# Kernel tuning notes

Measured on AMD Instinct MI355X. Metric: run time of the kernel, lower is better.

## Reference

```python
import jax, jax.numpy as jnp
import numpy as np

N, E, B = 50000, 800000, 16
IN_DIM, ED, HD, SD, NC = 64, 8, 128, 128, 8
T_STEPS = (8 + 16) // 2  # eval mode: (t_min + t_max) // 2 = 12


def setup_inputs() -> dict:
    key = jax.random.key(0)
    ks = jax.random.split(key, 12)
    s = 0.05  # small init scale so 12 residual steps stay bounded
    return {
        "x": jax.random.normal(ks[0], (N, IN_DIM), jnp.float32),
        "edge_index": jax.random.randint(ks[1], (2, E), 0, N, jnp.int64),
        "edge_attr": jax.random.normal(ks[2], (E, ED), jnp.float32),
        "batch": jnp.sort(jax.random.randint(ks[3], (N,), 0, B, jnp.int64)),
        "enc_w": jax.random.normal(ks[4], (IN_DIM, SD), jnp.float32) * s,
        "enc_b": jnp.zeros((SD,), jnp.float32),
        "msg_w": jax.random.normal(ks[5], (SD + ED, HD), jnp.float32) * s,
        "msg_b": jnp.zeros((HD,), jnp.float32),
        "up_w1": jax.random.normal(ks[6], (SD + HD, HD), jnp.float32) * s,
        "up_b1": jnp.zeros((HD,), jnp.float32),
        "up_w2": jax.random.normal(ks[7], (HD, SD), jnp.float32) * s,
        "up_b2": jnp.zeros((SD,), jnp.float32),
    }


def reference(x, edge_index, edge_attr, batch, enc_w, enc_b, msg_w, msg_b,
              up_w1, up_b1, up_w2, up_b2):
    src, dst = edge_index[0], edge_index[1]  # x_j = x[src], aggregate at dst
    # in-degree for mean aggregation (zero-degree nodes get 0, clamp avoids /0)
    deg = jax.ops.segment_sum(jnp.ones((E,), x.dtype), dst, num_segments=N)
    deg = jnp.clip(deg, 1.0)[:, None]

    # Encoder: Linear + ReLU
    state = jax.nn.relu(x @ enc_w + enc_b)  # [N, SD]

    for _ in range(T_STEPS):
        # message: relu(W_msg @ [h_j || e_ji])
        m = jax.nn.relu(jnp.concatenate([state[src], edge_attr], axis=-1) @ msg_w + msg_b)  # [E, HD]
        agg = jax.ops.segment_sum(m, dst, num_segments=N) / deg  # scatter-mean [N, HD]
        # update MLP on [h_i || m_bar_i]
        h = jax.nn.relu(jnp.concatenate([state, agg], axis=-1) @ up_w1 + up_b1)
        delta = h @ up_w2 + up_b2
        state = state + delta  # eval: no stochastic mask, no noise

    # Readout: per-graph mean over class channels
    class_ch = state[:, -NC:]  # [N, NC]
    cnt = jax.ops.segment_sum(jnp.ones((N,), x.dtype), batch, num_segments=B)
    logits = jax.ops.segment_sum(class_ch, batch, num_segments=B) / jnp.clip(cnt, 1.0)[:, None]
    return logits
```

## Files before the change

kernel.cpp:

```cpp
#include <hip/hip_runtime.h>
#include <hip/hip_bf16.h>

#define NN 50000
#define NE 800000
#define NB 16
#define T_STEPS 12
#define SCAN_B 196
#define EAW_BLOCKS 2048

typedef __attribute__((ext_vector_type(8))) short short8;
typedef __attribute__((ext_vector_type(4))) float f32x4;
typedef __attribute__((ext_vector_type(2))) float f32x2;
typedef unsigned short u16;
typedef unsigned int u32;

__device__ __forceinline__ float bf2f(u32 u) {
    union { u32 i; float f; } v; v.i = u << 16; return v.f;
}
__device__ __forceinline__ u16 f2bf(float f) {
    union { float f; u32 i; } v; v.f = f;
    u32 r = v.i + 0x7fffu + ((v.i >> 16) & 1u);
    return (u16)(r >> 16);
}
__device__ __forceinline__ f32x4 mfma16(short8 a, short8 b, f32x4 c) {
    return __builtin_amdgcn_mfma_f32_16x16x32_bf16(a, b, c, 0, 0, 0);
}

__device__ __forceinline__ u32 pk2_fp8(float o0, float o1) {
#if __has_builtin(__builtin_amdgcn_cvt_pk_fp8_f32)
    return (u32)__builtin_amdgcn_cvt_pk_fp8_f32(o0, o1, 0, false);
#else
    u32 a = 0;
    asm("v_cvt_pk_fp8_f32 %0, %1, %2" : "+v"(a) : "v"(o0), "v"(o1));
    return a;
#endif
}
__device__ __forceinline__ u32 pk4_fp8(float o0, float o1, float o2, float o3) {
    return (pk2_fp8(o0, o1) & 0xffffu) | (pk2_fp8(o2, o3) << 16);
}

__device__ __forceinline__ void fp8x4f(u32 w, float& f0, float& f1, float& f2, float& f3) {
#if __has_builtin(__builtin_amdgcn_cvt_pk_f32_fp8)
    f32x2 r0 = __builtin_amdgcn_cvt_pk_f32_fp8((int)w, false);
    f32x2 r1 = __builtin_amdgcn_cvt_pk_f32_fp8((int)w, true);
    f0 = r0[0]; f1 = r0[1]; f2 = r1[0]; f3 = r1[1];
#else
    f32x2 r0, r1;
    u32 hi = w >> 16;
    asm("v_cvt_pk_f32_fp8 %0, %1" : "=v"(r0) : "v"(w));
    asm("v_cvt_pk_f32_fp8 %0, %1" : "=v"(r1) : "v"(hi));
    f0 = r0[0]; f1 = r0[1]; f2 = r1[0]; f3 = r1[1];
#endif
}

#define W1OFF 0
#define W2OFF 32768
#define WSOFF 49152
#define ENCOFF 65536
#define PACKN 73728


__global__ void k_hist(const int* __restrict__ dst, int* __restrict__ hist) {
    int e = blockIdx.x * 256 + threadIdx.x;
    if (e < NE) atomicAdd(&hist[dst[e]], 1);
}

__global__ void k_scanA(const int* __restrict__ hist, int* __restrict__ excl,
                        int* __restrict__ bsum) {
    __shared__ int sh[256];
    int t = threadIdx.x, b = blockIdx.x;
    int idx = b * 256 + t;
    int v = (idx < NN) ? hist[idx] : 0;
    sh[t] = v;
    __syncthreads();
    for (int off = 1; off < 256; off <<= 1) {
        int add = (t >= off) ? sh[t - off] : 0;
        __syncthreads();
        sh[t] += add;
        __syncthreads();
    }
    if (idx < NN) excl[idx] = sh[t] - v;
    if (t == 255) bsum[b] = sh[255];
}

__global__ void k_scanB(int* __restrict__ bsum) {
    __shared__ int sh[256];
    int t = threadIdx.x;
    int v = (t < SCAN_B) ? bsum[t] : 0;
    sh[t] = v;
    __syncthreads();
    for (int off = 1; off < 256; off <<= 1) {
        int add = (t >= off) ? sh[t - off] : 0;
        __syncthreads();
        sh[t] += add;
        __syncthreads();
    }
    if (t < SCAN_B) bsum[t] = sh[t] - v;
}

__global__ void k_scanC(const int* __restrict__ excl, const int* __restrict__ bsum,
                        int* __restrict__ rowptr, int* __restrict__ cursor) {
    int idx = blockIdx.x * 256 + threadIdx.x;
    if (idx < NN) {
        int r = excl[idx] + bsum[blockIdx.x];
        rowptr[idx] = r;
        cursor[idx] = r;
    }
    if (idx == 0) rowptr[NN] = NE;
}

__global__ void k_scatter(const int* __restrict__ src, const int* __restrict__ dst,
                          const float* __restrict__ eattr, int* __restrict__ cursor,
                          int* __restrict__ ssrc, u16* __restrict__ ea8) {
    int e = blockIdx.x * 256 + threadIdx.x;
    if (e >= NE) return;
    int d = dst[e];
    int pos = atomicAdd(&cursor[d], 1);
    ssrc[pos] = src[e];
    const float* ap = eattr + (size_t)e * 8;
    uint4 w;
    w.x = (u32)f2bf(ap[0]) | ((u32)f2bf(ap[1]) << 16);
    w.y = (u32)f2bf(ap[2]) | ((u32)f2bf(ap[3]) << 16);
    w.z = (u32)f2bf(ap[4]) | ((u32)f2bf(ap[5]) << 16);
    w.w = (u32)f2bf(ap[6]) | ((u32)f2bf(ap[7]) << 16);
    *(uint4*)(ea8 + (size_t)pos * 8) = w;
}

__global__ __launch_bounds__(256) void k_eaw(
    const u16* __restrict__ ea8, const float* __restrict__ msg_w,
    unsigned char* __restrict__ eaw) {
    const int tid = threadIdx.x;
    const int hex = tid & 15;
    const int esub = tid >> 4;
    float w[8][8];
#pragma unroll
    for (int k = 0; k < 8; ++k) {
        float4 v0 = *(const float4*)(msg_w + (size_t)(128 + k) * 128 + hex * 8);
        float4 v1 = *(const float4*)(msg_w + (size_t)(128 + k) * 128 + hex * 8 + 4);
        w[k][0] = v0.x; w[k][1] = v0.y; w[k][2] = v0.z; w[k][3] = v0.w;
        w[k][4] = v1.x; w[k][5] = v1.y; w[k][6] = v1.z; w[k][7] = v1.w;
    }
    int p = blockIdx.x * 16 + esub;
    if (p >= NE) return;
    uint4 ev = *(const uint4*)(ea8 + (size_t)p * 8);
    while (true) {
        int pn = p + EAW_BLOCKS * 16;
        bool more = pn < NE;
        uint4 evn;
        if (more) evn = *(const uint4*)(ea8 + (size_t)pn * 8);
        float ef[8];
        ef[0] = bf2f(ev.x & 0xffffu); ef[1] = bf2f(ev.x >> 16);
        ef[2] = bf2f(ev.y & 0xffffu); ef[3] = bf2f(ev.y >> 16);
        ef[4] = bf2f(ev.z & 0xffffu); ef[5] = bf2f(ev.z >> 16);
        ef[6] = bf2f(ev.w & 0xffffu); ef[7] = bf2f(ev.w >> 16);
        float o[8];
#pragma unroll
        for (int c = 0; c < 8; ++c) o[c] = ef[0] * w[0][c];
#pragma unroll
        for (int k = 1; k < 8; ++k)
#pragma unroll
            for (int c = 0; c < 8; ++c) o[c] += ef[k] * w[k][c];
        uint2 q;
        q.x = pk4_fp8(o[0], o[1], o[2], o[3]);
        q.y = pk4_fp8(o[4], o[5], o[6], o[7]);
        *(uint2*)(eaw + (size_t)p * 128 + hex * 8) = q;
        if (!more) break;
        p = pn;
        ev = evn;
    }
}

__global__ void k_pack(const float* __restrict__ up_w1, const float* __restrict__ up_w2,
                       const float* __restrict__ msg_w, const float* __restrict__ enc_w,
                       u16* __restrict__ packed) {
    int idx = blockIdx.x * 256 + threadIdx.x;
    if (idx >= PACKN) return;
    const float* srcp; int local;
    if (idx < W2OFF)        { srcp = up_w1; local = idx; }
    else if (idx < WSOFF)   { srcp = up_w2; local = idx - W2OFF; }
    else if (idx < ENCOFF)  { srcp = msg_w; local = idx - WSOFF; }
    else                    { srcp = enc_w; local = idx - ENCOFF; }
    int j = local & 7;
    int l = (local >> 3) & 63;
    int ntks = local >> 9;
    int nt = ntks & 7;
    int ks = ntks >> 3;
    int krow = ks * 32 + (l >> 4) * 8 + j;
    int col = nt * 16 + (l & 15);
    packed[idx] = f2bf(srcp[krow * 128 + col]);
}


__global__ __launch_bounds__(256) void k_encode(
    const float* __restrict__ x, const float* __restrict__ enc_b,
    const float* __restrict__ msg_b, const u16* __restrict__ packed,
    float* __restrict__ state_f, u16* __restrict__ state_h, u16* __restrict__ swb) {
    __shared__ u16 stage[4][2048];
    const int wv = threadIdx.x >> 6, l = threadIdx.x & 63;
    const int lr = l & 15, kb = l >> 4;
    const int rb = blockIdx.x * 64 + wv * 16;
    const int row = rb + lr;
    const int rowc = row < NN ? row : NN - 1;

    f32x4 acc[8] = {};
#pragma unroll
    for (int ks = 0; ks < 2; ++ks) {
        const float* ap = x + (size_t)rowc * 64 + ks * 32 + kb * 8;
        float4 a0 = *(const float4*)ap;
        float4 a1 = *(const float4*)(ap + 4);
        short8 a;
        a[0] = (short)f2bf(a0.x); a[1] = (short)f2bf(a0.y);
        a[2] = (short)f2bf(a0.z); a[3] = (short)f2bf(a0.w);
        a[4] = (short)f2bf(a1.x); a[5] = (short)f2bf(a1.y);
        a[6] = (short)f2bf(a1.z); a[7] = (short)f2bf(a1.w);
        const u16* bp = packed + ENCOFF + (size_t)(ks * 512 + l) * 8;
#pragma unroll
        for (int nt = 0; nt < 8; ++nt) {
            short8 b = *(const short8*)(bp + nt * 512);
            acc[nt] = mfma16(a, b, acc[nt]);
        }
    }
#pragma unroll
    for (int nt = 0; nt < 8; ++nt) {
        int col = nt * 16 + lr;
        float bias = enc_b[col];
#pragma unroll
        for (int j = 0; j < 4; ++j) {
            int rl = kb * 4 + j;
            int r = rb + rl;
            float v = acc[nt][j] + bias;
            v = v > 0.f ? v : 0.f;
            u16 h = f2bf(v);
            if (r < NN) {
                state_f[(size_t)r * 128 + col] = v;
                state_h[(size_t)r * 128 + col] = h;
            }
            int byte = (rl * 256 + col * 2) ^ ((rl & 7) << 4);
            *(u16*)((char*)stage[wv] + byte) = h;
        }
    }
    f32x4 acc3[8] = {};
#pragma unroll
    for (int ks = 0; ks < 4; ++ks) {
        int byte = (lr * 256 + ks * 64 + kb * 16) ^ ((lr & 7) << 4);
        short8 a = *(const short8*)((char*)stage[wv] + byte);
        const u16* bp = packed + WSOFF + (size_t)(ks * 512 + l) * 8;
#pragma unroll
        for (int nt = 0; nt < 8; ++nt) {
            short8 b = *(const short8*)(bp + nt * 512);
            acc3[nt] = mfma16(a, b, acc3[nt]);
        }
    }
#pragma unroll
    for (int nt = 0; nt < 8; ++nt) {
        int col = nt * 16 + lr;
        float bias = msg_b[col];
#pragma unroll
        for (int j = 0; j < 4; ++j) {
            int r = rb + kb * 4 + j;
            if (r < NN) swb[(size_t)r * 128 + col] = f2bf(acc3[nt][j] + bias);
        }
    }
}


__global__ __launch_bounds__(256) void k_edge(
    const int* __restrict__ rowptr, const int* __restrict__ ssrc,
    const unsigned char* __restrict__ eaw, const u16* __restrict__ swb,
    u16* __restrict__ aggb) {
    __shared__ float red[4][2][4][129];
    const int wv = threadIdx.x >> 6, l = threadIdx.x & 63;
    const int half = l >> 5;
    const int slot = (l >> 3) & 3;
    const int g = l & 7;
    const int n = blockIdx.x * 8 + wv * 2 + half;
    if (n >= NN) return;
    const int e0 = rowptr[n], e1 = rowptr[n + 1];
    float acc[16];
#pragma unroll
    for (int c = 0; c < 16; ++c) acc[c] = 0.f;

    int i = e0 + slot;
    int s = (i < e1) ? ssrc[i] : 0;
    while (i < e1) {
        int inext = i + 4;
        int snext = (inext < e1) ? ssrc[inext] : 0;
        uint4 q = *(const uint4*)(eaw + (size_t)i * 128 + g * 16);
        const u16* sp = swb + (size_t)s * 128 + g * 16;
        uint4 sa = *(const uint4*)sp;
        uint4 sb = *(const uint4*)(sp + 8);
        float ef[16];
        fp8x4f(q.x, ef[0], ef[1], ef[2], ef[3]);
        fp8x4f(q.y, ef[4], ef[5], ef[6], ef[7]);
        fp8x4f(q.z, ef[8], ef[9], ef[10], ef[11]);
        fp8x4f(q.w, ef[12], ef[13], ef[14], ef[15]);
        u32 sw[8] = {sa.x, sa.y, sa.z, sa.w, sb.x, sb.y, sb.z, sb.w};
#pragma unroll
        for (int h = 0; h < 8; ++h) {
            union { u32 i; float f; } vlo, vhi;
            vlo.i = sw[h] << 16;
            vhi.i = sw[h] & 0xffff0000u;
            float m0 = vlo.f + ef[2 * h];
            float m1 = vhi.f + ef[2 * h + 1];
            acc[2 * h]     += m0 > 0.f ? m0 : 0.f;
            acc[2 * h + 1] += m1 > 0.f ? m1 : 0.f;
        }
        i = inext;
        s = snext;
    }
    float* rp = &red[wv][half][slot][g * 16];
#pragma unroll
    for (int c = 0; c < 16; c += 4) {
        f32x4 v = {acc[c], acc[c + 1], acc[c + 2], acc[c + 3]};
        *(f32x4*)(rp + c) = v;
    }
    const int lo = l & 31;
    const int ch = lo * 4;
    f32x4 sum = *(const f32x4*)&red[wv][half][0][ch];
#pragma unroll
    for (int sl = 1; sl < 4; ++sl) {
        f32x4 v = *(const f32x4*)&red[wv][half][sl][ch];
        sum[0] += v[0]; sum[1] += v[1]; sum[2] += v[2]; sum[3] += v[3];
    }
    int dg = e1 - e0;
    float inv = 1.f / (float)(dg > 0 ? dg : 1);
    uint2 outw;
    outw.x = (u32)f2bf(sum[0] * inv) | ((u32)f2bf(sum[1] * inv) << 16);
    outw.y = (u32)f2bf(sum[2] * inv) | ((u32)f2bf(sum[3] * inv) << 16);
    *(uint2*)(aggb + (size_t)n * 128 + ch) = outw;
}


__global__ __launch_bounds__(256) void k_update(
    const float* __restrict__ up_b1, const float* __restrict__ up_b2,
    const float* __restrict__ msg_b, const u16* __restrict__ packed,
    const u16* __restrict__ aggb, float* __restrict__ state_f,
    u16* __restrict__ state_h, u16* __restrict__ swb) {
    __shared__ u16 stage[4][2][2048];
    const int wv = threadIdx.x >> 6, l = threadIdx.x & 63;
    const int lr = l & 15, kb = l >> 4;
    const int rbase = blockIdx.x * 128 + wv * 32;

    f32x4 acc[2][8] = {};
#pragma unroll
    for (int ks = 0; ks < 8; ++ks) {
        short8 a[2];
#pragma unroll
        for (int rt = 0; rt < 2; ++rt) {
            int row = rbase + rt * 16 + lr;
            int rowc = row < NN ? row : NN - 1;
            const u16* abase = (ks < 4)
                ? (state_h + (size_t)rowc * 128 + ks * 32 + kb * 8)
                : (aggb + (size_t)rowc * 128 + (ks - 4) * 32 + kb * 8);
            a[rt] = *(const short8*)abase;
        }
        const u16* bp = packed + W1OFF + (size_t)(ks * 512 + l) * 8;
#pragma unroll
        for (int nt = 0; nt < 8; ++nt) {
            short8 b = *(const short8*)(bp + nt * 512);
            acc[0][nt] = mfma16(a[0], b, acc[0][nt]);
            acc[1][nt] = mfma16(a[1], b, acc[1][nt]);
        }
    }
#pragma unroll
    for (int nt = 0; nt < 8; ++nt) {
        int col = nt * 16 + lr;
        float b1v = up_b1[col];
#pragma unroll
        for (int rt = 0; rt < 2; ++rt) {
#pragma unroll
            for (int j = 0; j < 4; ++j) {
                int rl = kb * 4 + j;
                float v = acc[rt][nt][j] + b1v;
                v = v > 0.f ? v : 0.f;
                int byte = (rl * 256 + col * 2) ^ ((rl & 7) << 4);
                *(u16*)((char*)stage[wv][rt] + byte) = f2bf(v);
            }
        }
    }
    f32x4 acc2[2][8] = {};
#pragma unroll
    for (int ks = 0; ks < 4; ++ks) {
        int byte = (lr * 256 + ks * 64 + kb * 16) ^ ((lr & 7) << 4);
        short8 a[2];
        a[0] = *(const short8*)((char*)stage[wv][0] + byte);
        a[1] = *(const short8*)((char*)stage[wv][1] + byte);
        const u16* bp = packed + W2OFF + (size_t)(ks * 512 + l) * 8;
#pragma unroll
        for (int nt = 0; nt < 8; ++nt) {
            short8 b = *(const short8*)(bp + nt * 512);
            acc2[0][nt] = mfma16(a[0], b, acc2[0][nt]);
            acc2[1][nt] = mfma16(a[1], b, acc2[1][nt]);
        }
    }
#pragma unroll
    for (int rt = 0; rt < 2; ++rt) {
#pragma unroll
        for (int nt = 0; nt < 8; ++nt) {
            int col = nt * 16 + lr;
            float b2v = up_b2[col];
#pragma unroll
            for (int j = 0; j < 4; ++j) {
                int rl = kb * 4 + j;
                int r = rbase + rt * 16 + rl;
                int rc = r < NN ? r : NN - 1;
                float snew = state_f[(size_t)rc * 128 + col] + acc2[rt][nt][j] + b2v;
                u16 hb = f2bf(snew);
                if (r < NN) {
                    state_f[(size_t)r * 128 + col] = snew;
                    state_h[(size_t)r * 128 + col] = hb;
                }
                int byte = (rl * 256 + col * 2) ^ ((rl & 7) << 4);
                *(u16*)((char*)stage[wv][rt] + byte) = hb;
            }
        }
    }
    f32x4 acc3[2][8] = {};
#pragma unroll
    for (int ks = 0; ks < 4; ++ks) {
        int byte = (lr * 256 + ks * 64 + kb * 16) ^ ((lr & 7) << 4);
        short8 a[2];
        a[0] = *(const short8*)((char*)stage[wv][0] + byte);
        a[1] = *(const short8*)((char*)stage[wv][1] + byte);
        const u16* bp = packed + WSOFF + (size_t)(ks * 512 + l) * 8;
#pragma unroll
        for (int nt = 0; nt < 8; ++nt) {
            short8 b = *(const short8*)(bp + nt * 512);
            acc3[0][nt] = mfma16(a[0], b, acc3[0][nt]);
            acc3[1][nt] = mfma16(a[1], b, acc3[1][nt]);
        }
    }
#pragma unroll
    for (int rt = 0; rt < 2; ++rt) {
#pragma unroll
        for (int nt = 0; nt < 8; ++nt) {
            int col = nt * 16 + lr;
            float bias = msg_b[col];
#pragma unroll
            for (int j = 0; j < 4; ++j) {
                int r = rbase + rt * 16 + kb * 4 + j;
                if (r < NN) swb[(size_t)r * 128 + col] = f2bf(acc3[rt][nt][j] + bias);
            }
        }
    }
}


__global__ void k_logits(const float* __restrict__ state_f, const int* __restrict__ batch,
                         float* __restrict__ out) {
    __shared__ float red[256];
    int b = blockIdx.x, t = threadIdx.x;
    int ch = t & 7, sub = t >> 3;
    int lo = 0, hi = NN;
    while (lo < hi) { int m = (lo + hi) >> 1; if (batch[m] < b) lo = m + 1; else hi = m; }
    int s0 = lo;
    lo = 0; hi = NN;
    while (lo < hi) { int m = (lo + hi) >> 1; if (batch[m] < b + 1) lo = m + 1; else hi = m; }
    int s1 = lo;
    float acc = 0.f;
    for (int n = s0 + sub; n < s1; n += 32)
        acc += state_f[(size_t)n * 128 + 120 + ch];
    red[t] = acc;
    __syncthreads();
    for (int off = 16; off >= 1; off >>= 1) {
        if (sub < off) red[t] += red[t + off * 8];
        __syncthreads();
    }
    if (sub == 0) {
        int c = s1 - s0;
        float cnt = (float)(c > 0 ? c : 1);
        out[b * 8 + ch] = red[ch] / cnt;
    }
}


extern "C" void kernel_launch(void* const* d_in, const int* in_sizes, int n_in,
                              void* d_out, int out_size, void* d_ws, size_t ws_size,
                              hipStream_t stream) {
    (void)in_sizes; (void)n_in;
    const float* x      = (const float*)d_in[0];
    const int*   eidx   = (const int*)d_in[1];
    const float* eattr  = (const float*)d_in[2];
    const int*   batch  = (const int*)d_in[3];
    const float* enc_w  = (const float*)d_in[4];
    const float* enc_b  = (const float*)d_in[5];
    const float* msg_w  = (const float*)d_in[6];
    const float* msg_b  = (const float*)d_in[7];
    const float* up_w1  = (const float*)d_in[8];
    const float* up_b1  = (const float*)d_in[9];
    const float* up_w2  = (const float*)d_in[10];
    const float* up_b2  = (const float*)d_in[11];
    const int* esrc = eidx;
    const int* edst = eidx + NE;

    char* p = (char*)d_ws;
    size_t off = 0;
    auto carve = [&](size_t bytes) -> char* {
        char* r = p + off;
        off += (bytes + 255) & ~(size_t)255;
        return r;
    };
    float* state_f = (float*)carve((size_t)NN * 128 * 4);
    u16* state_h   = (u16*)carve((size_t)NN * 128 * 2);
    u16* aggb      = (u16*)carve((size_t)NN * 128 * 2);
    u16* swb       = (u16*)carve((size_t)NN * 128 * 2);
    int* ssrc      = (int*)carve((size_t)NE * 4);
    u16* ea8       = (u16*)carve((size_t)NE * 8 * 2);
    unsigned char* eaw = (unsigned char*)carve((size_t)NE * 128);
    int* rowptr    = (int*)carve((size_t)(NN + 1) * 4);
    int* cursor    = (int*)carve((size_t)NN * 4);
    int* hist      = (int*)carve((size_t)NN * 4);
    int* sexcl     = (int*)carve((size_t)NN * 4);
    int* bsum      = (int*)carve((size_t)256 * 4);
    u16* packed    = (u16*)carve((size_t)PACKN * 2);
    if (off > ws_size) {
        hipMemsetAsync(d_out, 0xFF, (size_t)out_size * 4, stream);
        return;
    }

    hipMemsetAsync(hist, 0, (size_t)NN * 4, stream);
    k_hist<<<(NE + 255) / 256, 256, 0, stream>>>(edst, hist);
    k_scanA<<<SCAN_B, 256, 0, stream>>>(hist, sexcl, bsum);
    k_scanB<<<1, 256, 0, stream>>>(bsum);
    k_scanC<<<SCAN_B, 256, 0, stream>>>(sexcl, bsum, rowptr, cursor);
    k_scatter<<<(NE + 255) / 256, 256, 0, stream>>>(esrc, edst, eattr, cursor, ssrc, ea8);
    k_eaw<<<EAW_BLOCKS, 256, 0, stream>>>(ea8, msg_w, eaw);
    k_pack<<<(PACKN + 255) / 256, 256, 0, stream>>>(up_w1, up_w2, msg_w, enc_w, packed);
    k_encode<<<(NN + 63) / 64, 256, 0, stream>>>(x, enc_b, msg_b, packed, state_f, state_h, swb);
    for (int t = 0; t < T_STEPS; ++t) {
        k_edge<<<(NN + 7) / 8, 256, 0, stream>>>(rowptr, ssrc, eaw, swb, aggb);
        k_update<<<(NN + 127) / 128, 256, 0, stream>>>(up_b1, up_b2, msg_b, packed, aggb,
                                                       state_f, state_h, swb);
    }
    k_logits<<<NB, 256, 0, stream>>>(state_f, batch, (float*)d_out);
}
```

Measured before the change: 1.211 ms.

## Drop fp32 state copy, keep residual in bf16, and prefetch edge loads one step ahead

```diff
diff --git a/kernel.cpp b/kernel.cpp
--- a/kernel.cpp
+++ b/kernel.cpp
@@ -194,7 +194,7 @@
 __global__ __launch_bounds__(256) void k_encode(
     const float* __restrict__ x, const float* __restrict__ enc_b,
     const float* __restrict__ msg_b, const u16* __restrict__ packed,
-    float* __restrict__ state_f, u16* __restrict__ state_h, u16* __restrict__ swb) {
+    u16* __restrict__ state_h, u16* __restrict__ swb) {
     __shared__ u16 stage[4][2048];
     const int wv = threadIdx.x >> 6, l = threadIdx.x & 63;
     const int lr = l & 15, kb = l >> 4;
@@ -231,10 +231,7 @@
             float v = acc[nt][j] + bias;
             v = v > 0.f ? v : 0.f;
             u16 h = f2bf(v);
-            if (r < NN) {
-                state_f[(size_t)r * 128 + col] = v;
-                state_h[(size_t)r * 128 + col] = h;
-            }
+            if (r < NN) state_h[(size_t)r * 128 + col] = h;
             int byte = (rl * 256 + col * 2) ^ ((rl & 7) << 4);
             *(u16*)((char*)stage[wv] + byte) = h;
         }
@@ -281,20 +278,32 @@
     for (int c = 0; c < 16; ++c) acc[c] = 0.f;
 
     int i = e0 + slot;
-    int s = (i < e1) ? ssrc[i] : 0;
+    uint4 qc = {0, 0, 0, 0}, sac = {0, 0, 0, 0}, sbc = {0, 0, 0, 0};
+    if (i < e1) {
+        int sc = ssrc[i];
+        qc = *(const uint4*)(eaw + (size_t)i * 128 + g * 16);
+        const u16* sp = swb + (size_t)sc * 128 + g * 16;
+        sac = *(const uint4*)sp;
+        sbc = *(const uint4*)(sp + 8);
+    }
+    int inext = i + 4;
+    int snext = (inext < e1) ? ssrc[inext] : 0;
     while (i < e1) {
-        int inext = i + 4;
-        int snext = (inext < e1) ? ssrc[inext] : 0;
-        uint4 q = *(const uint4*)(eaw + (size_t)i * 128 + g * 16);
-        const u16* sp = swb + (size_t)s * 128 + g * 16;
-        uint4 sa = *(const uint4*)sp;
-        uint4 sb = *(const uint4*)(sp + 8);
+        int i2 = inext + 4;
+        int s2 = (i2 < e1) ? ssrc[i2] : 0;
+        uint4 qn = {0, 0, 0, 0}, san = {0, 0, 0, 0}, sbn = {0, 0, 0, 0};
+        if (inext < e1) {
+            qn = *(const uint4*)(eaw + (size_t)inext * 128 + g * 16);
+            const u16* sp = swb + (size_t)snext * 128 + g * 16;
+            san = *(const uint4*)sp;
+            sbn = *(const uint4*)(sp + 8);
+        }
         float ef[16];
-        fp8x4f(q.x, ef[0], ef[1], ef[2], ef[3]);
-        fp8x4f(q.y, ef[4], ef[5], ef[6], ef[7]);
-        fp8x4f(q.z, ef[8], ef[9], ef[10], ef[11]);
-        fp8x4f(q.w, ef[12], ef[13], ef[14], ef[15]);
-        u32 sw[8] = {sa.x, sa.y, sa.z, sa.w, sb.x, sb.y, sb.z, sb.w};
+        fp8x4f(qc.x, ef[0], ef[1], ef[2], ef[3]);
+        fp8x4f(qc.y, ef[4], ef[5], ef[6], ef[7]);
+        fp8x4f(qc.z, ef[8], ef[9], ef[10], ef[11]);
+        fp8x4f(qc.w, ef[12], ef[13], ef[14], ef[15]);
+        u32 sw[8] = {sac.x, sac.y, sac.z, sac.w, sbc.x, sbc.y, sbc.z, sbc.w};
 #pragma unroll
         for (int h = 0; h < 8; ++h) {
             union { u32 i; float f; } vlo, vhi;
@@ -305,8 +314,10 @@
             acc[2 * h]     += m0 > 0.f ? m0 : 0.f;
             acc[2 * h + 1] += m1 > 0.f ? m1 : 0.f;
         }
+        qc = qn; sac = san; sbc = sbn;
         i = inext;
-        s = snext;
+        inext = i2;
+        snext = s2;
     }
     float* rp = &red[wv][half][slot][g * 16];
 #pragma unroll
@@ -334,8 +345,8 @@
 __global__ __launch_bounds__(256) void k_update(
     const float* __restrict__ up_b1, const float* __restrict__ up_b2,
     const float* __restrict__ msg_b, const u16* __restrict__ packed,
-    const u16* __restrict__ aggb, float* __restrict__ state_f,
-    u16* __restrict__ state_h, u16* __restrict__ swb) {
+    const u16* __restrict__ aggb, u16* __restrict__ state_h,
+    u16* __restrict__ swb) {
     __shared__ u16 stage[4][2][2048];
     const int wv = threadIdx.x >> 6, l = threadIdx.x & 63;
     const int lr = l & 15, kb = l >> 4;
@@ -404,12 +415,10 @@
                 int rl = kb * 4 + j;
                 int r = rbase + rt * 16 + rl;
                 int rc = r < NN ? r : NN - 1;
-                float snew = state_f[(size_t)rc * 128 + col] + acc2[rt][nt][j] + b2v;
+                float sold = bf2f((u32)state_h[(size_t)rc * 128 + col]);
+                float snew = sold + acc2[rt][nt][j] + b2v;
                 u16 hb = f2bf(snew);
-                if (r < NN) {
-                    state_f[(size_t)r * 128 + col] = snew;
-                    state_h[(size_t)r * 128 + col] = hb;
-                }
+                if (r < NN) state_h[(size_t)r * 128 + col] = hb;
                 int byte = (rl * 256 + col * 2) ^ ((rl & 7) << 4);
                 *(u16*)((char*)stage[wv][rt] + byte) = hb;
             }
@@ -446,7 +455,7 @@
 }
 
 
-__global__ void k_logits(const float* __restrict__ state_f, const int* __restrict__ batch,
+__global__ void k_logits(const u16* __restrict__ state_h, const int* __restrict__ batch,
                          float* __restrict__ out) {
     __shared__ float red[256];
     int b = blockIdx.x, t = threadIdx.x;
@@ -459,7 +468,7 @@
     int s1 = lo;
     float acc = 0.f;
     for (int n = s0 + sub; n < s1; n += 32)
-        acc += state_f[(size_t)n * 128 + 120 + ch];
+        acc += bf2f((u32)state_h[(size_t)n * 128 + 120 + ch]);
     red[t] = acc;
     __syncthreads();
     for (int off = 16; off >= 1; off >>= 1) {
@@ -500,7 +509,6 @@
         off += (bytes + 255) & ~(size_t)255;
         return r;
     };
-    float* state_f = (float*)carve((size_t)NN * 128 * 4);
     u16* state_h   = (u16*)carve((size_t)NN * 128 * 2);
     u16* aggb      = (u16*)carve((size_t)NN * 128 * 2);
     u16* swb       = (u16*)carve((size_t)NN * 128 * 2);
@@ -526,11 +534,11 @@
     k_scatter<<<(NE + 255) / 256, 256, 0, stream>>>(esrc, edst, eattr, cursor, ssrc, ea8);
     k_eaw<<<EAW_BLOCKS, 256, 0, stream>>>(ea8, msg_w, eaw);
     k_pack<<<(PACKN + 255) / 256, 256, 0, stream>>>(up_w1, up_w2, msg_w, enc_w, packed);
-    k_encode<<<(NN + 63) / 64, 256, 0, stream>>>(x, enc_b, msg_b, packed, state_f, state_h, swb);
+    k_encode<<<(NN + 63) / 64, 256, 0, stream>>>(x, enc_b, msg_b, packed, state_h, swb);
     for (int t = 0; t < T_STEPS; ++t) {
         k_edge<<<(NN + 7) / 8, 256, 0, stream>>>(rowptr, ssrc, eaw, swb, aggb);
         k_update<<<(NN + 127) / 128, 256, 0, stream>>>(up_b1, up_b2, msg_b, packed, aggb,
-                                                       state_f, state_h, swb);
-    }
-    k_logits<<<NB, 256, 0, stream>>>(state_f, batch, (float*)d_out);
-}
+                                                       state_h, swb);
+    }
+    k_logits<<<NB, 256, 0, stream>>>(state_h, batch, (float*)d_out);
+}
```

After: 1.135 ms. 1.07x faster.
